# Kernel tuning notes

Measured on AMD Instinct MI355X. Metric: run time of the kernel, lower is better.

Reference implementation:

```python
import jax, jax.numpy as jnp
import numpy as np

ALPHA = 0.9
EPS = 0.01
LAMBDA_PENALTY = 1.0
THRESHOLD = 0.8
COS_EPS = 1e-8
N, F, E = 8192, 256, 262144


def setup_inputs() -> dict:
    key = jax.random.key(0)
    k1, k2, k3, k4, k5 = jax.random.split(key, 5)
    z = jax.random.normal(k1, (N, F), dtype=jnp.float32)
    x_hat = jax.random.normal(k2, (N, F), dtype=jnp.float32)
    edge_index = jax.random.randint(k3, (2, E), 0, N, dtype=jnp.int64)
    f_k2u = jax.random.randint(k4, (N,), 0, 6, dtype=jnp.int64)
    f_u2k = jax.random.randint(k5, (N,), 0, 32, dtype=jnp.int64)
    return {"z": z, "x_hat": x_hat, "edge_index": edge_index,
            "f_k2u": f_k2u, "f_u2k": f_u2k, "epoch": 10}


def _corrcoef_features(z):
    # torch.corrcoef(z.T): correlation between the F feature columns over N nodes
    zm = z - jnp.mean(z, axis=0, keepdims=True)        # [N, F]
    cov = zm.T @ zm                                    # [F, F] (scale cancels in corr)
    std = jnp.sqrt(jnp.diag(cov))                      # [F]
    cor = cov / (std[:, None] * std[None, :])
    cor = jnp.clip(jnp.nan_to_num(cor), -1.0, 1.0)
    # fill_diagonal_(0)
    return cor * (1.0 - jnp.eye(cor.shape[0], dtype=cor.dtype))


def reference(z, x_hat, edge_index, f_k2u, f_u2k, epoch):
    n, f = z.shape
    zm = z - jnp.mean(z, axis=0, keepdims=True)
    cor = _corrcoef_features(z)                        # [F, F]
    # per-node scalar weight: alpha**f_k2u + (1 - alpha**f_u2k)
    w = (ALPHA ** f_k2u.astype(z.dtype)
         + (1.0 - ALPHA ** f_u2k.astype(z.dtype)))     # [N]
    W = w[:, None] * zm                                # [N, F]
    z2 = z + EPS * (W @ cor)                           # [N, F]

    # homophily (crash=True): per-edge cosine sim, scatter-add by source, degree-normalize
    i, j = edge_index[0], edge_index[1]
    zi, zj = z2[i], z2[j]                              # [E, F] gathers
    num = jnp.sum(zi * zj, axis=1)
    ni = jnp.maximum(jnp.linalg.norm(zi, axis=1), COS_EPS)
    nj = jnp.maximum(jnp.linalg.norm(zj, axis=1), COS_EPS)
    sim = num / (ni * nj)                              # [E]
    scores = jax.ops.segment_sum(sim, i, num_segments=n)
    deg = jax.ops.segment_sum(jnp.ones_like(sim), i, num_segments=n)
    deg = jnp.where(deg == 0, 1.0, deg)
    homophily_loss = -jnp.mean(scores / deg)

    # extra_loss (crash=True): dense NxN similarity masked by dense adjacency
    sim_mat = z2 @ z2.T                                # [N, N]
    adj = jnp.zeros((n, n), dtype=z.dtype)
    adj = adj.at[i, j].set(1.0).at[j, i].set(1.0)
    non_conn = sim_mat * (1.0 - adj)
    penalty = jnp.mean(jnp.where(non_conn > THRESHOLD, non_conn, 0.0))

    return homophily_loss + LAMBDA_PENALTY * penalty
```

## Files before the change

### kernel.cpp

```cpp
#include <hip/hip_runtime.h>
#include <stdint.h>
#include <math.h>

#define EPS_C 0.01f
#define THRESH 0.8f

constexpr int Nn = 8192;
constexpr int Ff = 256;
constexpr int Ee = 262144;

__device__ __forceinline__ float b2f(unsigned short u) {
  union { uint32_t i; float f; } v; v.i = ((uint32_t)u) << 16; return v.f;
}
__device__ __forceinline__ unsigned short f2b(float f) {
  union { uint32_t i; float f; } v; v.f = f;
  uint32_t r = v.i + 0x7FFFu + ((v.i >> 16) & 1u);
  return (unsigned short)(r >> 16);
}

typedef __bf16 bf16x8 __attribute__((ext_vector_type(8)));
typedef float f32x4 __attribute__((ext_vector_type(4)));

__global__ void k_transpose(const float* __restrict__ z, unsigned short* __restrict__ zT,
                            float* __restrict__ colsum) {
  __shared__ float Ls[64][65];
  int n0 = blockIdx.x * 64;
  int c0 = blockIdx.y * 64;
  int t = threadIdx.x;
  int r = t >> 4;
  int cq = t & 15;
#pragma unroll
  for (int i = 0; i < 4; ++i) {
    int row = r + 16 * i;
    float4 v = *(const float4*)(z + (size_t)(n0 + row) * Ff + c0 + cq * 4);
    Ls[row][cq * 4 + 0] = v.x;
    Ls[row][cq * 4 + 1] = v.y;
    Ls[row][cq * 4 + 2] = v.z;
    Ls[row][cq * 4 + 3] = v.w;
  }
  __syncthreads();
  if (t < 64) {
    float s = 0.f;
#pragma unroll
    for (int rr = 0; rr < 64; ++rr) s += Ls[rr][t];
    atomicAdd(&colsum[c0 + t], s);
  }
  int cr = t >> 4;
  int nq = t & 15;
#pragma unroll
  for (int i = 0; i < 4; ++i) {
    int c = cr + 16 * i;
    ushort4 o;
    o.x = f2b(Ls[nq * 4 + 0][c]);
    o.y = f2b(Ls[nq * 4 + 1][c]);
    o.z = f2b(Ls[nq * 4 + 2][c]);
    o.w = f2b(Ls[nq * 4 + 3][c]);
    *(ushort4*)(zT + (size_t)(c0 + c) * Nn + n0 + nq * 4) = o;
  }
}

__global__ __launch_bounds__(256, 2) void k_covg(const unsigned short* __restrict__ zT,
                                                 float* __restrict__ covp) {
  int bx = blockIdx.x, by = blockIdx.y, p = blockIdx.z;
  __shared__ __align__(16) unsigned short As[128 * 64];
  __shared__ __align__(16) unsigned short Bs[128 * 64];
  int t = threadIdx.x;
  int lane = t & 63, wv = t >> 6;
  int wr = wv >> 1, wc = wv & 1;
  int quad = lane >> 4, l15 = lane & 15;
  int a0 = by * 128, b0 = bx * 128;

  f32x4 acc[4][4];
#pragma unroll
  for (int i = 0; i < 4; ++i)
#pragma unroll
    for (int j = 0; j < 4; ++j) acc[i][j] = (f32x4){0.f, 0.f, 0.f, 0.f};

  for (int kk = 0; kk < 8; ++kk) {
    int k0 = p * 512 + kk * 64;
#pragma unroll
    for (int it = 0; it < 4; ++it) {
      int s = it * 256 + t;
      int r = s >> 3;
      int g = (s & 7) ^ (r & 7);
      const unsigned short* ga = zT + (size_t)(a0 + r) * Nn + k0 + g * 8;
      const unsigned short* gb = zT + (size_t)(b0 + r) * Nn + k0 + g * 8;
      __builtin_amdgcn_global_load_lds((const __attribute__((address_space(1))) void*)ga,
                                       (__attribute__((address_space(3))) void*)(As + s * 8),
                                       16, 0, 0);
      __builtin_amdgcn_global_load_lds((const __attribute__((address_space(1))) void*)gb,
                                       (__attribute__((address_space(3))) void*)(Bs + s * 8),
                                       16, 0, 0);
    }
    __syncthreads();
#pragma unroll
    for (int kc = 0; kc < 2; ++kc) {
      bf16x8 afr[4], bfr[4];
#pragma unroll
      for (int mt = 0; mt < 4; ++mt) {
        int rA = wr * 64 + mt * 16 + l15;
        int g = kc * 4 + quad;
        int gl = g ^ (rA & 7);
        afr[mt] = *(const bf16x8*)(As + ((size_t)rA * 8 + gl) * 8);
      }
#pragma unroll
      for (int nt = 0; nt < 4; ++nt) {
        int rB = wc * 64 + nt * 16 + l15;
        int g = kc * 4 + quad;
        int gl = g ^ (rB & 7);
        bfr[nt] = *(const bf16x8*)(Bs + ((size_t)rB * 8 + gl) * 8);
      }
#pragma unroll
      for (int mt = 0; mt < 4; ++mt)
#pragma unroll
        for (int nt = 0; nt < 4; ++nt)
          acc[mt][nt] = __builtin_amdgcn_mfma_f32_16x16x32_bf16(afr[mt], bfr[nt],
                                                                acc[mt][nt], 0, 0, 0);
    }
    __syncthreads();
  }

  float* outp = covp + (size_t)p * 65536;
#pragma unroll
  for (int mt = 0; mt < 4; ++mt)
#pragma unroll
    for (int r = 0; r < 4; ++r) {
      int a = a0 + wr * 64 + mt * 16 + quad * 4 + r;
#pragma unroll
      for (int nt = 0; nt < 4; ++nt) {
        int b = b0 + wc * 64 + nt * 16 + l15;
        outp[(size_t)a * Ff + b] = acc[mt][nt][r];
      }
    }
}

__global__ void k_cor(const float* __restrict__ covp, const float* __restrict__ colsum,
                      float* __restrict__ cor) {
  __shared__ float sd[256];
  int a = blockIdx.x, b = threadIdx.x;
  float mb = colsum[b] * (1.f / 8192.f);
  float gb = 0.f;
#pragma unroll
  for (int p = 0; p < 16; ++p) gb += covp[(size_t)p * 65536 + b * 257];
  float sb = sqrtf(gb - 8192.f * mb * mb);
  sd[b] = sb;
  float g = 0.f;
#pragma unroll
  for (int p = 0; p < 16; ++p) g += covp[(size_t)p * 65536 + a * Ff + b];
  __syncthreads();
  float c = 0.f;
  if (a != b) {
    float ma = colsum[a] * (1.f / 8192.f);
    float cv = g - 8192.f * ma * mb;
    c = cv / (sd[a] * sb);
    if (c != c) c = 0.f;
    c = fminf(1.f, fmaxf(-1.f, c));
  }
  cor[a * Ff + b] = c;
}

__global__ __launch_bounds__(256) void k_z2(const float* __restrict__ z,
    const float* __restrict__ colsum, const int* __restrict__ k2u,
    const int* __restrict__ u2k, const float* __restrict__ cor,
    unsigned short* __restrict__ z2b, float* __restrict__ norms) {
  __shared__ float Wl[32 * 256];
  __shared__ float ws_[32];
  int t = threadIdx.x;
  int row0 = blockIdx.x * 32;
  if (t < 32) {
    int row = row0 + t;
    ws_[t] = powf(0.9f, (float)k2u[row]) + 1.f - powf(0.9f, (float)u2k[row]);
  }
  __syncthreads();
  float mt = colsum[t] * (1.f / 8192.f);
  for (int rr = 0; rr < 32; ++rr) {
    int row = row0 + rr;
    Wl[rr * 256 + t] = ws_[rr] * (z[(size_t)row * Ff + t] - mt);
  }
  __syncthreads();
  int tc = t & 63, tr = t >> 6;
  float acc[8][4];
#pragma unroll
  for (int i = 0; i < 8; ++i)
#pragma unroll
    for (int j = 0; j < 4; ++j) acc[i][j] = 0.f;
  const float* corc = cor + tc * 4;
  for (int k = 0; k < 256; ++k) {
    float4 c4 = *(const float4*)(corc + (size_t)k * 256);
#pragma unroll
    for (int rr = 0; rr < 8; ++rr) {
      float wv = Wl[(tr * 8 + rr) * 256 + k];
      acc[rr][0] = fmaf(wv, c4.x, acc[rr][0]);
      acc[rr][1] = fmaf(wv, c4.y, acc[rr][1]);
      acc[rr][2] = fmaf(wv, c4.z, acc[rr][2]);
      acc[rr][3] = fmaf(wv, c4.w, acc[rr][3]);
    }
  }
#pragma unroll
  for (int rr = 0; rr < 8; ++rr) {
    int row = row0 + tr * 8 + rr;
    float4 zv = *(const float4*)(z + (size_t)row * Ff + tc * 4);
    float x0 = zv.x + EPS_C * acc[rr][0];
    float x1 = zv.y + EPS_C * acc[rr][1];
    float x2 = zv.z + EPS_C * acc[rr][2];
    float x3 = zv.w + EPS_C * acc[rr][3];
    ushort4 o;
    o.x = f2b(x0); o.y = f2b(x1); o.z = f2b(x2); o.w = f2b(x3);
    *(ushort4*)(z2b + (size_t)row * Ff + tc * 4) = o;
    float s = x0 * x0 + x1 * x1 + x2 * x2 + x3 * x3;
#pragma unroll
    for (int m = 1; m < 64; m <<= 1) s += __shfl_xor(s, m);
    if (tc == 0) norms[row] = fmaxf(sqrtf(s), 1e-8f);
  }
}

__global__ void k_adj(const int* __restrict__ ei, const int* __restrict__ ej,
                      unsigned int* __restrict__ adj) {
  int e = blockIdx.x * 256 + threadIdx.x;
  unsigned int i = (unsigned int)ei[e], j = (unsigned int)ej[e];
  size_t b1 = (size_t)i * Nn + j;
  size_t b2 = (size_t)j * Nn + i;
  atomicOr(&adj[b1 >> 5], 1u << (b1 & 31));
  atomicOr(&adj[b2 >> 5], 1u << (b2 & 31));
}

__global__ __launch_bounds__(256) void k_edge(const int* __restrict__ ei,
                       const int* __restrict__ ej,
                       const unsigned short* __restrict__ z2b,
                       const float* __restrict__ norms,
                       float* __restrict__ scores, float* __restrict__ deg) {
  int t = threadIdx.x;
  int wv = t >> 6, lane = t & 63;
  int half = lane >> 5;
  int l32 = lane & 31;
  int gw = blockIdx.x * 4 + wv;
  int ebase = gw * 32;
#pragma unroll 2
  for (int it = 0; it < 16; ++it) {
    int e = ebase + it * 2 + half;
    int i = ei[e], j = ej[e];
    uint4 ua = *(const uint4*)(z2b + (size_t)i * Ff + l32 * 8);
    uint4 ub = *(const uint4*)(z2b + (size_t)j * Ff + l32 * 8);
    float d = 0.f;
    const uint32_t* pa = (const uint32_t*)&ua;
    const uint32_t* pb = (const uint32_t*)&ub;
#pragma unroll
    for (int q = 0; q < 4; ++q) {
      union { uint32_t u; float f; } alo, ahi, blo, bhi;
      alo.u = pa[q] << 16;  ahi.u = pa[q] & 0xffff0000u;
      blo.u = pb[q] << 16;  bhi.u = pb[q] & 0xffff0000u;
      d = fmaf(alo.f, blo.f, d);
      d = fmaf(ahi.f, bhi.f, d);
    }
#pragma unroll
    for (int m = 1; m < 32; m <<= 1) d += __shfl_xor(d, m);
    if (l32 == 0) {
      float sim = d / (norms[i] * norms[j]);
      atomicAdd(&scores[i], sim);
      atomicAdd(&deg[i], 1.f);
    }
  }
}

__global__ __launch_bounds__(256, 2) void k_penalty(const unsigned short* __restrict__ z2b,
    const unsigned int* __restrict__ adj, double* __restrict__ psum) {
  int tb = blockIdx.x;
  int br = (int)(64.5 - sqrt(64.5 * 64.5 - 2.0 * (double)tb));
  while ((br + 1) * 64 - ((br + 1) * br) / 2 <= tb) ++br;
  while (br * 64 - (br * (br - 1)) / 2 > tb) --br;
  int bc = br + (tb - (br * 64 - (br * (br - 1)) / 2));

  __shared__ __align__(16) unsigned short LB[32768];
  int t = threadIdx.x;
  int lane = t & 63;
  int wv = t >> 6;
  int wr = wv >> 1, wc = wv & 1;
  int quad = lane >> 4;
  int l15 = lane & 15;
  int arow0 = br * 128, brow0 = bc * 128;

  f32x4 acc[4][4];
#pragma unroll
  for (int i = 0; i < 4; ++i)
#pragma unroll
    for (int j = 0; j < 4; ++j) acc[i][j] = (f32x4){0.f, 0.f, 0.f, 0.f};

#define ISSUE_PHASE(p)                                                                   \
  {                                                                                      \
    unsigned short* buf = LB + ((p) & 1) * 16384;                                        \
    int k0 = (p) * 64;                                                                   \
    _Pragma("unroll")                                                                    \
    for (int it = 0; it < 4; ++it) {                                                     \
      int s = it * 256 + t;                                                              \
      int r = s >> 3;                                                                    \
      int g = (s & 7) ^ (r & 7);                                                         \
      const unsigned short* ga = z2b + (size_t)(arow0 + r) * Ff + k0 + g * 8;            \
      const unsigned short* gb = z2b + (size_t)(brow0 + r) * Ff + k0 + g * 8;            \
      __builtin_amdgcn_global_load_lds((const __attribute__((address_space(1))) void*)ga,\
                                       (__attribute__((address_space(3))) void*)(buf + s * 8),      \
                                       16, 0, 0);                                        \
      __builtin_amdgcn_global_load_lds((const __attribute__((address_space(1))) void*)gb,\
                                       (__attribute__((address_space(3))) void*)(buf + 8192 + s * 8),\
                                       16, 0, 0);                                        \
    }                                                                                    \
  }

  ISSUE_PHASE(0)
  ISSUE_PHASE(1)
#pragma unroll
  for (int p = 0; p < 4; ++p) {
    if (p < 3) __builtin_amdgcn_s_waitcnt(0xF78);
    else       __builtin_amdgcn_s_waitcnt(0xF70);
    __builtin_amdgcn_s_barrier();
    const unsigned short* As = LB + (p & 1) * 16384;
    const unsigned short* Bs = As + 8192;
#pragma unroll
    for (int kc = 0; kc < 2; ++kc) {
      bf16x8 afr[4], bfr[4];
#pragma unroll
      for (int mt = 0; mt < 4; ++mt) {
        int rA = wr * 64 + mt * 16 + l15;
        int g = kc * 4 + quad;
        int gl = g ^ (rA & 7);
        afr[mt] = *(const bf16x8*)(As + ((size_t)rA * 8 + gl) * 8);
      }
#pragma unroll
      for (int nt = 0; nt < 4; ++nt) {
        int rB = wc * 64 + nt * 16 + l15;
        int g = kc * 4 + quad;
        int gl = g ^ (rB & 7);
        bfr[nt] = *(const bf16x8*)(Bs + ((size_t)rB * 8 + gl) * 8);
      }
#pragma unroll
      for (int mt = 0; mt < 4; ++mt)
#pragma unroll
        for (int nt = 0; nt < 4; ++nt)
          acc[mt][nt] = __builtin_amdgcn_mfma_f32_16x16x32_bf16(afr[mt], bfr[nt],
                                                                acc[mt][nt], 0, 0, 0);
    }
    __builtin_amdgcn_s_barrier();
    if (p < 2) ISSUE_PHASE(p + 2)
  }
#undef ISSUE_PHASE

  float local = 0.f;
  int a_base = arow0 + wr * 64;
  int b_base = brow0 + wc * 64;
#pragma unroll
  for (int mt = 0; mt < 4; ++mt) {
#pragma unroll
    for (int r = 0; r < 4; ++r) {
      int a = a_base + mt * 16 + quad * 4 + r;
      uint64_t bits = *(const uint64_t*)(adj + (size_t)a * 256 + (b_base >> 5));
#pragma unroll
      for (int nt = 0; nt < 4; ++nt) {
        float v = acc[mt][nt][r];
        int boff = nt * 16 + l15;
        bool conn = (bits >> boff) & 1ull;
        float wgt;
        if (br != bc) wgt = 2.f;
        else {
          int b = b_base + boff;
          wgt = (a < b) ? 2.f : (a == b ? 1.f : 0.f);
        }
        if (!conn && v > THRESH) local += wgt * v;
      }
    }
  }
#pragma unroll
  for (int m = 1; m < 64; m <<= 1) local += __shfl_xor(local, m);
  __syncthreads();
  float* red = (float*)LB;
  if (lane == 0) red[wv] = local;
  __syncthreads();
  if (t == 0) atomicAdd(psum, (double)(red[0] + red[1] + red[2] + red[3]));
}

__global__ void k_final(const float* __restrict__ scores, const float* __restrict__ deg,
                        const double* __restrict__ psum, float* __restrict__ out) {
  __shared__ float red[4];
  int t = threadIdx.x;
  float acc = 0.f;
#pragma unroll 4
  for (int it = 0; it < 32; ++it) {
    int n = it * 256 + t;
    float dg = deg[n];
    acc += scores[n] / (dg == 0.f ? 1.f : dg);
  }
#pragma unroll
  for (int m = 1; m < 64; m <<= 1) acc += __shfl_xor(acc, m);
  if ((t & 63) == 0) red[t >> 6] = acc;
  __syncthreads();
  if (t == 0) {
    double h = -(double)(red[0] + red[1] + red[2] + red[3]) / 8192.0;
    double p = (*psum) / (8192.0 * 8192.0);
    out[0] = (float)(h + p);
  }
}

extern "C" void kernel_launch(void* const* d_in, const int* in_sizes, int n_in,
                              void* d_out, int out_size, void* d_ws, size_t ws_size,
                              hipStream_t stream) {
  const float* z = (const float*)d_in[0];
  const int* ei = (const int*)d_in[2];
  const int* ej = ei + Ee;
  const int* k2u = (const int*)d_in[3];
  const int* u2k = (const int*)d_in[4];

  char* ws = (char*)d_ws;
  unsigned int* adj = (unsigned int*)(ws);
  float* colsum     = (float*)(ws + 8388608);
  float* scores     = (float*)(ws + 8389632);
  float* deg        = (float*)(ws + 8422400);
  double* psum      = (double*)(ws + 8455168);
  const size_t ZERO_BYTES = 8455176;
  float* covp       = (float*)(ws + 8455296);
  unsigned short* zT  = (unsigned short*)(ws + 12649600);
  unsigned short* z2b = (unsigned short*)(ws + 16843904);
  float* cor        = (float*)(ws + 21038208);
  float* norms      = (float*)(ws + 21300352);

  hipMemsetAsync(d_ws, 0, ZERO_BYTES, stream);
  k_adj<<<1024, 256, 0, stream>>>(ei, ej, adj);
  k_transpose<<<dim3(128, 4), 256, 0, stream>>>(z, zT, colsum);
  k_covg<<<dim3(2, 2, 16), 256, 0, stream>>>(zT, covp);
  k_cor<<<256, 256, 0, stream>>>(covp, colsum, cor);
  k_z2<<<256, 256, 0, stream>>>(z, colsum, k2u, u2k, cor, z2b, norms);
  k_edge<<<2048, 256, 0, stream>>>(ei, ej, z2b, norms, scores, deg);
  k_penalty<<<2080, 256, 0, stream>>>(z2b, adj, psum);
  k_final<<<1, 256, 0, stream>>>(scores, deg, psum, (float*)d_out);
}
```

Measured before the change: 224.6 us.

## Load MFMA fragments directly from global memory instead of staging through LDS

Both the covariance GEMM and the NxN penalty GEMM stop staging tiles in LDS with global_load_lds, swizzling and barriers. Each lane now reads its bf16x8 fragments straight from global memory (relying on L1/L2 for reuse), and the block-level LDS reduction becomes per-wave double atomics. This removes LDS traffic, barriers and shared-memory occupancy limits, but gives up explicit reuse and the double-buffered prefetch, so fragment loads are repeated across waves and coalescing is poorer.

```diff
diff --git a/kernel.cpp b/kernel.cpp
--- a/kernel.cpp
+++ b/kernel.cpp
@@ -59,16 +59,16 @@
   }
 }
 
-__global__ __launch_bounds__(256, 2) void k_covg(const unsigned short* __restrict__ zT,
-                                                 float* __restrict__ covp) {
+__global__ __launch_bounds__(256) void k_covg(const unsigned short* __restrict__ zT,
+                                              float* __restrict__ covp) {
   int bx = blockIdx.x, by = blockIdx.y, p = blockIdx.z;
-  __shared__ __align__(16) unsigned short As[128 * 64];
-  __shared__ __align__(16) unsigned short Bs[128 * 64];
   int t = threadIdx.x;
   int lane = t & 63, wv = t >> 6;
   int wr = wv >> 1, wc = wv & 1;
   int quad = lane >> 4, l15 = lane & 15;
   int a0 = by * 128, b0 = bx * 128;
+  const unsigned short* Ab = zT + (size_t)(a0 + wr * 64 + l15) * Nn;
+  const unsigned short* Bb = zT + (size_t)(b0 + wc * 64 + l15) * Nn;
 
   f32x4 acc[4][4];
 #pragma unroll
@@ -76,48 +76,22 @@
 #pragma unroll
     for (int j = 0; j < 4; ++j) acc[i][j] = (f32x4){0.f, 0.f, 0.f, 0.f};
 
-  for (int kk = 0; kk < 8; ++kk) {
-    int k0 = p * 512 + kk * 64;
-#pragma unroll
-    for (int it = 0; it < 4; ++it) {
-      int s = it * 256 + t;
-      int r = s >> 3;
-      int g = (s & 7) ^ (r & 7);
-      const unsigned short* ga = zT + (size_t)(a0 + r) * Nn + k0 + g * 8;
-      const unsigned short* gb = zT + (size_t)(b0 + r) * Nn + k0 + g * 8;
-      __builtin_amdgcn_global_load_lds((const __attribute__((address_space(1))) void*)ga,
-                                       (__attribute__((address_space(3))) void*)(As + s * 8),
-                                       16, 0, 0);
-      __builtin_amdgcn_global_load_lds((const __attribute__((address_space(1))) void*)gb,
-                                       (__attribute__((address_space(3))) void*)(Bs + s * 8),
-                                       16, 0, 0);
-    }
-    __syncthreads();
-#pragma unroll
-    for (int kc = 0; kc < 2; ++kc) {
-      bf16x8 afr[4], bfr[4];
-#pragma unroll
-      for (int mt = 0; mt < 4; ++mt) {
-        int rA = wr * 64 + mt * 16 + l15;
-        int g = kc * 4 + quad;
-        int gl = g ^ (rA & 7);
-        afr[mt] = *(const bf16x8*)(As + ((size_t)rA * 8 + gl) * 8);
-      }
-#pragma unroll
-      for (int nt = 0; nt < 4; ++nt) {
-        int rB = wc * 64 + nt * 16 + l15;
-        int g = kc * 4 + quad;
-        int gl = g ^ (rB & 7);
-        bfr[nt] = *(const bf16x8*)(Bs + ((size_t)rB * 8 + gl) * 8);
-      }
-#pragma unroll
-      for (int mt = 0; mt < 4; ++mt)
-#pragma unroll
-        for (int nt = 0; nt < 4; ++nt)
-          acc[mt][nt] = __builtin_amdgcn_mfma_f32_16x16x32_bf16(afr[mt], bfr[nt],
-                                                                acc[mt][nt], 0, 0, 0);
-    }
-    __syncthreads();
+#pragma unroll 4
+  for (int ks = 0; ks < 16; ++ks) {
+    int koff = p * 512 + ks * 32 + quad * 8;
+    bf16x8 afr[4], bfr[4];
+#pragma unroll
+    for (int mt = 0; mt < 4; ++mt)
+      afr[mt] = *(const bf16x8*)(Ab + (size_t)mt * 16 * Nn + koff);
+#pragma unroll
+    for (int nt = 0; nt < 4; ++nt)
+      bfr[nt] = *(const bf16x8*)(Bb + (size_t)nt * 16 * Nn + koff);
+#pragma unroll
+    for (int mt = 0; mt < 4; ++mt)
+#pragma unroll
+      for (int nt = 0; nt < 4; ++nt)
+        acc[mt][nt] = __builtin_amdgcn_mfma_f32_16x16x32_bf16(afr[mt], bfr[nt],
+                                                              acc[mt][nt], 0, 0, 0);
   }
 
   float* outp = covp + (size_t)p * 65536;
@@ -262,7 +236,7 @@
   }
 }
 
-__global__ __launch_bounds__(256, 2) void k_penalty(const unsigned short* __restrict__ z2b,
+__global__ __launch_bounds__(256) void k_penalty(const unsigned short* __restrict__ z2b,
     const unsigned int* __restrict__ adj, double* __restrict__ psum) {
   int tb = blockIdx.x;
   int br = (int)(64.5 - sqrt(64.5 * 64.5 - 2.0 * (double)tb));
@@ -270,7 +244,6 @@
   while (br * 64 - (br * (br - 1)) / 2 > tb) --br;
   int bc = br + (tb - (br * 64 - (br * (br - 1)) / 2));
 
-  __shared__ __align__(16) unsigned short LB[32768];
   int t = threadIdx.x;
   int lane = t & 63;
   int wv = t >> 6;
@@ -278,6 +251,8 @@
   int quad = lane >> 4;
   int l15 = lane & 15;
   int arow0 = br * 128, brow0 = bc * 128;
+  const unsigned short* Ab = z2b + (size_t)(arow0 + wr * 64 + l15) * Ff;
+  const unsigned short* Bb = z2b + (size_t)(brow0 + wc * 64 + l15) * Ff;
 
   f32x4 acc[4][4];
 #pragma unroll
@@ -285,63 +260,23 @@
 #pragma unroll
     for (int j = 0; j < 4; ++j) acc[i][j] = (f32x4){0.f, 0.f, 0.f, 0.f};
 
-#define ISSUE_PHASE(p)                                                                   \
-  {                                                                                      \
-    unsigned short* buf = LB + ((p) & 1) * 16384;                                        \
-    int k0 = (p) * 64;                                                                   \
-    _Pragma("unroll")                                                                    \
-    for (int it = 0; it < 4; ++it) {                                                     \
-      int s = it * 256 + t;                                                              \
-      int r = s >> 3;                                                                    \
-      int g = (s & 7) ^ (r & 7);                                                         \
-      const unsigned short* ga = z2b + (size_t)(arow0 + r) * Ff + k0 + g * 8;            \
-      const unsigned short* gb = z2b + (size_t)(brow0 + r) * Ff + k0 + g * 8;            \
-      __builtin_amdgcn_global_load_lds((const __attribute__((address_space(1))) void*)ga,\
-                                       (__attribute__((address_space(3))) void*)(buf + s * 8),      \
-                                       16, 0, 0);                                        \
-      __builtin_amdgcn_global_load_lds((const __attribute__((address_space(1))) void*)gb,\
-                                       (__attribute__((address_space(3))) void*)(buf + 8192 + s * 8),\
-                                       16, 0, 0);                                        \
-    }                                                                                    \
-  }
-
-  ISSUE_PHASE(0)
-  ISSUE_PHASE(1)
-#pragma unroll
-  for (int p = 0; p < 4; ++p) {
-    if (p < 3) __builtin_amdgcn_s_waitcnt(0xF78);
-    else       __builtin_amdgcn_s_waitcnt(0xF70);
-    __builtin_amdgcn_s_barrier();
-    const unsigned short* As = LB + (p & 1) * 16384;
-    const unsigned short* Bs = As + 8192;
-#pragma unroll
-    for (int kc = 0; kc < 2; ++kc) {
-      bf16x8 afr[4], bfr[4];
-#pragma unroll
-      for (int mt = 0; mt < 4; ++mt) {
-        int rA = wr * 64 + mt * 16 + l15;
-        int g = kc * 4 + quad;
-        int gl = g ^ (rA & 7);
-        afr[mt] = *(const bf16x8*)(As + ((size_t)rA * 8 + gl) * 8);
-      }
-#pragma unroll
-      for (int nt = 0; nt < 4; ++nt) {
-        int rB = wc * 64 + nt * 16 + l15;
-        int g = kc * 4 + quad;
-        int gl = g ^ (rB & 7);
-        bfr[nt] = *(const bf16x8*)(Bs + ((size_t)rB * 8 + gl) * 8);
-      }
-#pragma unroll
-      for (int mt = 0; mt < 4; ++mt)
-#pragma unroll
-        for (int nt = 0; nt < 4; ++nt)
-          acc[mt][nt] = __builtin_amdgcn_mfma_f32_16x16x32_bf16(afr[mt], bfr[nt],
-                                                                acc[mt][nt], 0, 0, 0);
-    }
-    __builtin_amdgcn_s_barrier();
-    if (p < 2) ISSUE_PHASE(p + 2)
-  }
-#undef ISSUE_PHASE
+#pragma unroll
+  for (int ks = 0; ks < 8; ++ks) {
+    int koff = ks * 32 + quad * 8;
+    bf16x8 afr[4], bfr[4];
+#pragma unroll
+    for (int mt = 0; mt < 4; ++mt)
+      afr[mt] = *(const bf16x8*)(Ab + (size_t)mt * 16 * Ff + koff);
+#pragma unroll
+    for (int nt = 0; nt < 4; ++nt)
+      bfr[nt] = *(const bf16x8*)(Bb + (size_t)nt * 16 * Ff + koff);
+#pragma unroll
+    for (int mt = 0; mt < 4; ++mt)
+#pragma unroll
+      for (int nt = 0; nt < 4; ++nt)
+        acc[mt][nt] = __builtin_amdgcn_mfma_f32_16x16x32_bf16(afr[mt], bfr[nt],
+                                                              acc[mt][nt], 0, 0, 0);
+  }
 
   float local = 0.f;
   int a_base = arow0 + wr * 64;
@@ -369,11 +304,7 @@
   }
 #pragma unroll
   for (int m = 1; m < 64; m <<= 1) local += __shfl_xor(local, m);
-  __syncthreads();
-  float* red = (float*)LB;
-  if (lane == 0) red[wv] = local;
-  __syncthreads();
-  if (t == 0) atomicAdd(psum, (double)(red[0] + red[1] + red[2] + red[3]));
+  if (lane == 0) atomicAdd(psum, (double)local);
 }
 
 __global__ void k_final(const float* __restrict__ scores, const float* __restrict__ deg,
```

After: 332.9 us. 48.3% more time.
